# Optimization experiments

Hardware: AMD Instinct MI355X
Metric: run time of the kernel (lower is better)

Reference implementation:

```python
import jax, jax.numpy as jnp
import numpy as np

WS = 8      # window_size
NH = 3      # num_heads
SHIFT = True
LN_EPS = 1e-5


def _ln(x, w, b):
    m = jnp.mean(x, axis=-1, keepdims=True)
    v = jnp.mean(jnp.square(x - m), axis=-1, keepdims=True)
    return (x - m) * jax.lax.rsqrt(v + LN_EPS) * w + b


def _window_partition(x):
    B, H, W, C = x.shape
    x = x.reshape(B, H // WS, WS, W // WS, WS, C)
    return x.transpose(0, 1, 3, 2, 4, 5).reshape(-1, WS * WS, C)


def _window_reverse(win, B, H, W):
    C = win.shape[-1]
    x = win.reshape(B, H // WS, W // WS, WS, WS, C)
    return x.transpose(0, 1, 3, 2, 4, 5).reshape(B, H, W, C)


def setup_inputs() -> dict:
    key = jax.random.key(0)
    ks = jax.random.split(key, 6)
    C = 96
    x = jax.random.normal(ks[0], (4, 224, 224, C), dtype=jnp.float32)
    return {
        "x": x,
        "ln1_w": jnp.ones((C,), jnp.float32),
        "ln1_b": jnp.zeros((C,), jnp.float32),
        "in_proj_w": jax.random.normal(ks[1], (3 * C, C), jnp.float32) * 0.02,
        "in_proj_b": jnp.zeros((3 * C,), jnp.float32),
        "out_proj_w": jax.random.normal(ks[2], (C, C), jnp.float32) * 0.02,
        "out_proj_b": jnp.zeros((C,), jnp.float32),
        "ln2_w": jnp.ones((C,), jnp.float32),
        "ln2_b": jnp.zeros((C,), jnp.float32),
        "mlp_w1": jax.random.normal(ks[3], (4 * C, C), jnp.float32) * 0.02,
        "mlp_b1": jnp.zeros((4 * C,), jnp.float32),
        "mlp_w2": jax.random.normal(ks[4], (C, 4 * C), jnp.float32) * 0.02,
        "mlp_b2": jnp.zeros((C,), jnp.float32),
    }


def reference(x, ln1_w, ln1_b, in_proj_w, in_proj_b, out_proj_w, out_proj_b,
              ln2_w, ln2_b, mlp_w1, mlp_b1, mlp_w2, mlp_b2):
    B, H, W, C = x.shape
    hd = C // NH
    s = WS // 2
    if SHIFT:
        x = jnp.roll(x, shift=(-s, -s), axis=(1, 2))
    xw = _window_partition(x)                      # [nw, WS*WS, C]
    h = _ln(xw, ln1_w, ln1_b)
    qkv = h @ in_proj_w.T + in_proj_b              # [nw, L, 3C]
    q, k, v = jnp.split(qkv, 3, axis=-1)
    nw, L = q.shape[0], q.shape[1]
    q = q.reshape(nw, L, NH, hd).transpose(0, 2, 1, 3)
    k = k.reshape(nw, L, NH, hd).transpose(0, 2, 1, 3)
    v = v.reshape(nw, L, NH, hd).transpose(0, 2, 1, 3)
    scores = jnp.einsum('whqd,whkd->whqk', q, k) * (1.0 / np.sqrt(hd))
    attn = jax.nn.softmax(scores, axis=-1)
    o = jnp.einsum('whqk,whkd->whqd', attn, v).transpose(0, 2, 1, 3).reshape(nw, L, C)
    o = o @ out_proj_w.T + out_proj_b
    x = _window_reverse(o, B, H, W)                # attention REPLACES x (no residual, per source)
    if SHIFT:
        x = jnp.roll(x, shift=(s, s), axis=(1, 2))
    h2 = _ln(x, ln2_w, ln2_b)
    mlp = jax.nn.gelu(h2 @ mlp_w1.T + mlp_b1, approximate=False) @ mlp_w2.T + mlp_b2
    return x + mlp
```

## Files before the change

### kernel.cpp

```cpp
#include <hip/hip_runtime.h>
#include <math.h>

static constexpr int Hn   = 224;
static constexpr int Wn   = 224;
static constexpr int Cn   = 96;
static constexpr int Sft  = 4;
static constexpr int NWH  = 28;
static constexpr int NWPB = 784;
static constexpr int NW   = 3136;

typedef __attribute__((ext_vector_type(8))) short bf16x8;
typedef __attribute__((ext_vector_type(4))) float f32x4;
typedef __attribute__((ext_vector_type(4))) short s16x4;

__device__ inline short f2bf(float f) {
    unsigned u = __float_as_uint(f);
    return (short)((u + 0x7fffu + ((u >> 16) & 1u)) >> 16);
}

__device__ inline float gelu_f(float a) {
    float u  = a * 0.70710678118654752f;
    float au = fabsf(u);
    float t  = __builtin_amdgcn_rcpf(fmaf(0.3275911f, au, 1.f));
    float e  = __expf(-u * u);
    float p  = t * fmaf(t, fmaf(t, fmaf(t, fmaf(t, 1.061405429f,
                        -1.453152027f), 1.421413741f), -0.284496736f),
                        0.254829592f);
    float er = fmaf(-p, e, 1.f);
    er = (u < 0.f) ? -er : er;
    return 0.5f * a * (1.f + er);
}

__global__ void prep_bf16(const float* __restrict__ wqkv, const float* __restrict__ wo,
                          const float* __restrict__ w1,   const float* __restrict__ w2,
                          short* __restrict__ ws) {
    int idx = blockIdx.x * 256 + threadIdx.x;
    if (idx < 27648)        ws[idx] = f2bf(wqkv[idx]);
    else if (idx < 36864)   ws[idx] = f2bf(wo[idx - 27648]);
    else if (idx < 73728)   ws[idx] = f2bf(w1[idx - 36864]);
    else if (idx < 110592)  ws[idx] = f2bf(w2[idx - 73728]);
}

static constexpr int LDH  = 104;
static constexpr int LDQK = 200;
static constexpr int LDVT = 72;
static constexpr int LDP  = 200;
static constexpr int LDXF = 100;
static constexpr int LDST = 100;
static constexpr int LDAQ = 104;

__global__ __launch_bounds__(256) __attribute__((amdgpu_waves_per_eu(4, 4)))
void attn_mlp(
    const float* __restrict__ x,
    const float* __restrict__ ln1w, const float* __restrict__ ln1b,
    const short* __restrict__ wqb,  const float* __restrict__ bqkv,
    const short* __restrict__ wob,  const float* __restrict__ bo,
    const float* __restrict__ ln2w, const float* __restrict__ ln2b,
    const short* __restrict__ w1b,  const float* __restrict__ b1,
    const short* __restrict__ w2b,  const float* __restrict__ b2,
    float* __restrict__ out)
{
    __shared__ __align__(16) char  A[64 * 400];
    __shared__ __align__(16) short Bsh[96 * LDVT];
    __shared__ int   tbase[64];

    const int blk = blockIdx.x;
    const int b   = blk / NWPB;
    const int rem = blk - b * NWPB;
    const int wh  = rem / NWH;
    const int ww  = rem - wh * NWH;
    const int tid  = threadIdx.x;
    const int lane = tid & 63;
    const int wv   = __builtin_amdgcn_readfirstlane(tid >> 6);
    const int lr   = lane & 15;
    const int lk   = lane >> 4;
    const int wr   = wv >> 1;
    const int wc   = wv & 1;

    if (tid < 64) {
        int i = tid >> 3, j = tid & 7;
        int hs = wh * 8 + i + Sft; if (hs >= Hn) hs -= Hn;
        int ws2 = ww * 8 + j + Sft; if (ws2 >= Wn) ws2 -= Wn;
        tbase[tid] = ((b * Hn + hs) * Wn + ws2) * Cn;
    }
    __syncthreads();

    float* xf = (float*)A;
    for (int i = tid; i < 64 * 24; i += 256) {
        int row = i / 24, c4 = i - row * 24;
        float4 v = ((const float4*)(x + tbase[row]))[c4];
        *(float4*)&xf[row * LDXF + c4 * 4] = v;
    }
    __syncthreads();

    {
        short* lnb = Bsh;
        const int l = tid >> 2, p = tid & 3;
        float s0 = 0.f, s1 = 0.f;
        #pragma unroll
        for (int c0 = 0; c0 < 24; ++c0) {
            float v = xf[l * LDXF + p * 24 + c0];
            s0 += v; s1 += v * v;
        }
        s0 += __shfl_xor(s0, 1); s1 += __shfl_xor(s1, 1);
        s0 += __shfl_xor(s0, 2); s1 += __shfl_xor(s1, 2);
        float mean = s0 * (1.f / 96.f);
        float var  = fmaxf(s1 * (1.f / 96.f) - mean * mean, 0.f);
        float rstd = rsqrtf(var + 1e-5f);
        #pragma unroll
        for (int c0 = 0; c0 < 24; ++c0) {
            int c = p * 24 + c0;
            float v = xf[l * LDXF + c];
            lnb[l * LDH + c] = f2bf((v - mean) * rstd * ln1w[c] + ln1b[c]);
        }
    }
    __syncthreads();

    short* qk = (short*)A;
    short* vt = Bsh;
    {
        bf16x8 aq[2][3];
        #pragma unroll
        for (int rt = 0; rt < 2; ++rt)
            #pragma unroll
            for (int ks = 0; ks < 3; ++ks)
                aq[rt][ks] = *(const bf16x8*)&Bsh[(wr * 32 + rt * 16 + lr) * LDH + ks * 32 + lk * 8];
        __syncthreads();

        #pragma unroll 3
        for (int ct9 = 0; ct9 < 9; ++ct9) {
            const int ct = wc * 9 + ct9;
            const short* bp = wqb + (ct * 16 + lr) * 96 + lk * 8;
            bf16x8 b0 = *(const bf16x8*)(bp);
            bf16x8 b1 = *(const bf16x8*)(bp + 32);
            bf16x8 b2v = *(const bf16x8*)(bp + 64);
            const int col  = ct * 16 + lr;
            const float bs = bqkv[col];
            #pragma unroll
            for (int rt = 0; rt < 2; ++rt) {
                f32x4 acc = (f32x4){0.f, 0.f, 0.f, 0.f};
                acc = __builtin_amdgcn_mfma_f32_16x16x32_bf16(aq[rt][0], b0, acc, 0, 0, 0);
                acc = __builtin_amdgcn_mfma_f32_16x16x32_bf16(aq[rt][1], b1, acc, 0, 0, 0);
                acc = __builtin_amdgcn_mfma_f32_16x16x32_bf16(aq[rt][2], b2v, acc, 0, 0, 0);
                const int rb = wr * 32 + rt * 16;
                if (ct < 12) {
                    #pragma unroll
                    for (int r = 0; r < 4; ++r)
                        qk[(rb + lk * 4 + r) * LDQK + col] = f2bf(acc[r] + bs);
                } else {
                    s16x4 pk;
                    #pragma unroll
                    for (int r = 0; r < 4; ++r) pk[r] = f2bf(acc[r] + bs);
                    *(s16x4*)&vt[(col - 192) * LDVT + rb + lk * 4] = pk;
                }
            }
        }
    }
    __syncthreads();

    short* pb = (short*)A;
    {
        f32x4 accs[3][4];
        #pragma unroll
        for (int h = 0; h < 3; ++h) {
            bf16x8 aqf = *(const bf16x8*)&qk[(wv * 16 + lr) * LDQK + h * 32 + lk * 8];
            #pragma unroll
            for (int ct = 0; ct < 4; ++ct) {
                bf16x8 bk = *(const bf16x8*)&qk[(ct * 16 + lr) * LDQK + 96 + h * 32 + lk * 8];
                f32x4 z = (f32x4){0.f, 0.f, 0.f, 0.f};
                accs[h][ct] = __builtin_amdgcn_mfma_f32_16x16x32_bf16(aqf, bk, z, 0, 0, 0);
            }
        }
        __syncthreads();

        const float scale = 0.17677669529663687f;
        float inv[3][4];
        #pragma unroll
        for (int h = 0; h < 3; ++h) {
            #pragma unroll
            for (int r = 0; r < 4; ++r) {
                float m = fmaxf(fmaxf(accs[h][0][r], accs[h][1][r]),
                                fmaxf(accs[h][2][r], accs[h][3][r]));
                m = fmaxf(m, __shfl_xor(m, 1));
                m = fmaxf(m, __shfl_xor(m, 2));
                m = fmaxf(m, __shfl_xor(m, 4));
                m = fmaxf(m, __shfl_xor(m, 8));
                float s = 0.f;
                #pragma unroll
                for (int ct = 0; ct < 4; ++ct) {
                    float p = __expf((accs[h][ct][r] - m) * scale);
                    accs[h][ct][r] = p; s += p;
                }
                s += __shfl_xor(s, 1); s += __shfl_xor(s, 2);
                s += __shfl_xor(s, 4); s += __shfl_xor(s, 8);
                inv[h][r] = 1.f / s;
            }
        }
        #pragma unroll
        for (int h = 0; h < 3; ++h)
            #pragma unroll
            for (int ct = 0; ct < 4; ++ct)
                #pragma unroll
                for (int r = 0; r < 4; ++r)
                    pb[(wv * 16 + lk * 4 + r) * LDP + h * 64 + ct * 16 + lr] =
                        f2bf(accs[h][ct][r]);

        f32x4 acco[3][2];
        #pragma unroll
        for (int h = 0; h < 3; ++h)
            #pragma unroll
            for (int ct = 0; ct < 2; ++ct) acco[h][ct] = (f32x4){0.f, 0.f, 0.f, 0.f};
        #pragma unroll
        for (int h = 0; h < 3; ++h) {
            #pragma unroll
            for (int ks = 0; ks < 2; ++ks) {
                bf16x8 ap = *(const bf16x8*)&pb[(wv * 16 + lr) * LDP + h * 64 + ks * 32 + lk * 8];
                #pragma unroll
                for (int ct = 0; ct < 2; ++ct) {
                    bf16x8 bv = *(const bf16x8*)&vt[(h * 32 + ct * 16 + lr) * LDVT + ks * 32 + lk * 8];
                    acco[h][ct] = __builtin_amdgcn_mfma_f32_16x16x32_bf16(ap, bv, acco[h][ct], 0, 0, 0);
                }
            }
        }
        #pragma unroll
        for (int h = 0; h < 3; ++h)
            #pragma unroll
            for (int ct = 0; ct < 2; ++ct)
                #pragma unroll
                for (int r = 0; r < 4; ++r)
                    pb[(wv * 16 + lk * 4 + r) * LDP + h * 32 + ct * 16 + lr] =
                        f2bf(acco[h][ct][r] * inv[h][r]);
    }

    float* st = (float*)A;
    {
        bf16x8 o0 = *(const bf16x8*)&pb[(wv * 16 + lr) * LDP +  0 + lk * 8];
        bf16x8 o1 = *(const bf16x8*)&pb[(wv * 16 + lr) * LDP + 32 + lk * 8];
        bf16x8 o2 = *(const bf16x8*)&pb[(wv * 16 + lr) * LDP + 64 + lk * 8];
        #pragma unroll
        for (int ct = 0; ct < 6; ++ct) {
            const short* bp = wob + (ct * 16 + lr) * 96 + lk * 8;
            bf16x8 b0 = *(const bf16x8*)(bp);
            bf16x8 b1 = *(const bf16x8*)(bp + 32);
            bf16x8 b2v = *(const bf16x8*)(bp + 64);
            f32x4 acc = (f32x4){0.f, 0.f, 0.f, 0.f};
            acc = __builtin_amdgcn_mfma_f32_16x16x32_bf16(o0, b0, acc, 0, 0, 0);
            acc = __builtin_amdgcn_mfma_f32_16x16x32_bf16(o1, b1, acc, 0, 0, 0);
            acc = __builtin_amdgcn_mfma_f32_16x16x32_bf16(o2, b2v, acc, 0, 0, 0);
            const int col = ct * 16 + lr;
            const float bs = bo[col];
            #pragma unroll
            for (int r = 0; r < 4; ++r)
                st[(wv * 16 + lk * 4 + r) * LDST + col] = acc[r] + bs;
        }
    }
    __syncthreads();

    {
        short* lnb = Bsh;
        const int l = tid >> 2, p = tid & 3;
        float s0 = 0.f, s1 = 0.f;
        #pragma unroll
        for (int c0 = 0; c0 < 24; ++c0) {
            float v = st[l * LDST + p * 24 + c0];
            s0 += v; s1 += v * v;
        }
        s0 += __shfl_xor(s0, 1); s1 += __shfl_xor(s1, 1);
        s0 += __shfl_xor(s0, 2); s1 += __shfl_xor(s1, 2);
        float mean = s0 * (1.f / 96.f);
        float var  = fmaxf(s1 * (1.f / 96.f) - mean * mean, 0.f);
        float rstd = rsqrtf(var + 1e-5f);
        #pragma unroll
        for (int c0 = 0; c0 < 24; ++c0) {
            int c = p * 24 + c0;
            float v = st[l * LDST + c];
            lnb[l * LDH + c] = f2bf((v - mean) * rstd * ln2w[c] + ln2b[c]);
        }
    }
    __syncthreads();

    short* actQ = Bsh;
    bf16x8 a1[4][3];
    #pragma unroll
    for (int rt = 0; rt < 4; ++rt)
        #pragma unroll
        for (int ks = 0; ks < 3; ++ks)
            a1[rt][ks] = *(const bf16x8*)&Bsh[(rt * 16 + lr) * LDH + ks * 32 + lk * 8];
    __syncthreads();

    for (int half = 0; half < 2; ++half) {
        const int oc0w = half * 192 + wv * 48;
        f32x4 acc1[4][3];
        #pragma unroll
        for (int rt = 0; rt < 4; ++rt)
            #pragma unroll
            for (int ct = 0; ct < 3; ++ct) acc1[rt][ct] = (f32x4){0.f, 0.f, 0.f, 0.f};

        #pragma unroll
        for (int ct = 0; ct < 3; ++ct) {
            const short* bp = w1b + (oc0w + ct * 16 + lr) * 96 + lk * 8;
            bf16x8 bg0 = *(const bf16x8*)(bp);
            bf16x8 bg1 = *(const bf16x8*)(bp + 32);
            bf16x8 bg2 = *(const bf16x8*)(bp + 64);
            #pragma unroll
            for (int rt = 0; rt < 4; ++rt) {
                acc1[rt][ct] = __builtin_amdgcn_mfma_f32_16x16x32_bf16(a1[rt][0], bg0, acc1[rt][ct], 0, 0, 0);
                acc1[rt][ct] = __builtin_amdgcn_mfma_f32_16x16x32_bf16(a1[rt][1], bg1, acc1[rt][ct], 0, 0, 0);
                acc1[rt][ct] = __builtin_amdgcn_mfma_f32_16x16x32_bf16(a1[rt][2], bg2, acc1[rt][ct], 0, 0, 0);
            }
        }

        for (int sub = 0; sub < 2; ++sub) {
            if (wr == sub) {
                #pragma unroll
                for (int ct = 0; ct < 3; ++ct) {
                    float bias = b1[oc0w + ct * 16 + lr];
                    const int lcol = wc * 48 + ct * 16 + lr;
                    #pragma unroll
                    for (int rt = 0; rt < 4; ++rt) {
                        #pragma unroll
                        for (int r = 0; r < 4; ++r) {
                            float g = gelu_f(acc1[rt][ct][r] + bias);
                            actQ[(rt * 16 + lk * 4 + r) * LDAQ + lcol] = f2bf(g);
                        }
                    }
                }
            }
            __syncthreads();

            {
                f32x4 ps[2][3];
                #pragma unroll
                for (int rt = 0; rt < 2; ++rt)
                    #pragma unroll
                    for (int ct = 0; ct < 3; ++ct) ps[rt][ct] = (f32x4){0.f, 0.f, 0.f, 0.f};

                #pragma unroll
                for (int ks = 0; ks < 3; ++ks) {
                    bf16x8 a2[2];
                    #pragma unroll
                    for (int rt = 0; rt < 2; ++rt)
                        a2[rt] = *(const bf16x8*)&actQ[(wr * 32 + rt * 16 + lr) * LDAQ + ks * 32 + lk * 8];
                    #pragma unroll
                    for (int ct = 0; ct < 3; ++ct) {
                        bf16x8 bw = *(const bf16x8*)(w2b + (wc * 48 + ct * 16 + lr) * 384
                                                      + half * 192 + sub * 96 + ks * 32 + lk * 8);
                        #pragma unroll
                        for (int rt = 0; rt < 2; ++rt)
                            ps[rt][ct] = __builtin_amdgcn_mfma_f32_16x16x32_bf16(a2[rt], bw, ps[rt][ct], 0, 0, 0);
                    }
                }

                const bool last = (half == 1) && (sub == 1);
                #pragma unroll
                for (int ct = 0; ct < 3; ++ct) {
                    const int col = wc * 48 + ct * 16 + lr;
                    const float addb = last ? b2[col] : 0.f;
                    #pragma unroll
                    for (int rt = 0; rt < 2; ++rt) {
                        #pragma unroll
                        for (int r = 0; r < 4; ++r) {
                            const int row = wr * 32 + rt * 16 + lk * 4 + r;
                            st[row * LDST + col] += ps[rt][ct][r] + addb;
                        }
                    }
                }
            }
            __syncthreads();
        }
    }

    for (int i = tid; i < 64 * 96; i += 256) {
        int l = i / 96, c = i - l * 96;
        out[tbase[l] + c] = st[l * LDST + c];
    }
}

extern "C" void kernel_launch(void* const* d_in, const int* in_sizes, int n_in,
                              void* d_out, int out_size, void* d_ws, size_t ws_size,
                              hipStream_t stream) {
    const float* x    = (const float*)d_in[0];
    const float* ln1w = (const float*)d_in[1];
    const float* ln1b = (const float*)d_in[2];
    const float* wqkv = (const float*)d_in[3];
    const float* bqkv = (const float*)d_in[4];
    const float* wo   = (const float*)d_in[5];
    const float* bo   = (const float*)d_in[6];
    const float* ln2w = (const float*)d_in[7];
    const float* ln2b = (const float*)d_in[8];
    const float* w1   = (const float*)d_in[9];
    const float* b1   = (const float*)d_in[10];
    const float* w2   = (const float*)d_in[11];
    const float* b2   = (const float*)d_in[12];
    float* out = (float*)d_out;

    short* ws  = (short*)d_ws;
    short* wqb = ws;
    short* wob = ws + 27648;
    short* w1b = ws + 36864;
    short* w2b = ws + 73728;

    prep_bf16<<<432, 256, 0, stream>>>(wqkv, wo, w1, w2, ws);
    attn_mlp<<<NW, 256, 0, stream>>>(x, ln1w, ln1b, wqb, bqkv, wob, bo,
                                     ln2w, ln2b, w1b, b1, w2b, b2, out);
}
```

Measured before the change: 223.6 us.

## Restructure MLP so each wave owns 16 rows, removing block barriers

The MLP stage now gives each wave its own 16 token rows and a private LDS scratch region. The wave computes the full fc1 output for 192 columns per half, applies GELU, and runs fc2 with register accumulators across both halves. This removes the shared activation buffer and the several __syncthreads per half, and adds the residual to st only once at the end. In exchange each wave reloads all W1 and W2 weights, so global and L2 weight traffic goes up fourfold. LDS grows and the launch bounds change from a fixed 4 waves per EU to a minimum of 3 blocks, which can change occupancy.

```diff
diff --git a/kernel.cpp b/kernel.cpp
--- a/kernel.cpp
+++ b/kernel.cpp
@@ -47,10 +47,9 @@
 static constexpr int LDP  = 200;
 static constexpr int LDXF = 100;
 static constexpr int LDST = 100;
-static constexpr int LDAQ = 104;
-
-__global__ __launch_bounds__(256) __attribute__((amdgpu_waves_per_eu(4, 4)))
-void attn_mlp(
+static constexpr int LDM  = 200;
+
+__global__ __launch_bounds__(256, 3) void attn_mlp(
     const float* __restrict__ x,
     const float* __restrict__ ln1w, const float* __restrict__ ln1b,
     const short* __restrict__ wqb,  const float* __restrict__ bqkv,
@@ -61,7 +60,7 @@
     float* __restrict__ out)
 {
     __shared__ __align__(16) char  A[64 * 400];
-    __shared__ __align__(16) short Bsh[96 * LDVT];
+    __shared__ __align__(16) short Bsh[12800];
     __shared__ int   tbase[64];
 
     const int blk = blockIdx.x;
@@ -256,9 +255,12 @@
     }
     __syncthreads();
 
-    {
-        short* lnb = Bsh;
-        const int l = tid >> 2, p = tid & 3;
+    short* Mw = Bsh + wv * (16 * LDM);
+
+    {
+        const int l   = tid >> 2;
+        const int lr2 = lane >> 2;
+        const int p   = tid & 3;
         float s0 = 0.f, s1 = 0.f;
         #pragma unroll
         for (int c0 = 0; c0 < 24; ++c0) {
@@ -274,101 +276,67 @@
         for (int c0 = 0; c0 < 24; ++c0) {
             int c = p * 24 + c0;
             float v = st[l * LDST + c];
-            lnb[l * LDH + c] = f2bf((v - mean) * rstd * ln2w[c] + ln2b[c]);
-        }
-    }
-    __syncthreads();
-
-    short* actQ = Bsh;
-    bf16x8 a1[4][3];
+            Mw[lr2 * LDM + c] = f2bf((v - mean) * rstd * ln2w[c] + ln2b[c]);
+        }
+    }
+
+    bf16x8 a1[3];
     #pragma unroll
-    for (int rt = 0; rt < 4; ++rt)
-        #pragma unroll
-        for (int ks = 0; ks < 3; ++ks)
-            a1[rt][ks] = *(const bf16x8*)&Bsh[(rt * 16 + lr) * LDH + ks * 32 + lk * 8];
-    __syncthreads();
+    for (int ks = 0; ks < 3; ++ks)
+        a1[ks] = *(const bf16x8*)&Mw[lr * LDM + ks * 32 + lk * 8];
+
+    f32x4 acc2[6];
+    #pragma unroll
+    for (int ct = 0; ct < 6; ++ct) acc2[ct] = (f32x4){0.f, 0.f, 0.f, 0.f};
 
     for (int half = 0; half < 2; ++half) {
-        const int oc0w = half * 192 + wv * 48;
-        f32x4 acc1[4][3];
-        #pragma unroll
-        for (int rt = 0; rt < 4; ++rt)
-            #pragma unroll
-            for (int ct = 0; ct < 3; ++ct) acc1[rt][ct] = (f32x4){0.f, 0.f, 0.f, 0.f};
-
-        #pragma unroll
-        for (int ct = 0; ct < 3; ++ct) {
-            const short* bp = w1b + (oc0w + ct * 16 + lr) * 96 + lk * 8;
+        f32x4 acc1[12];
+        #pragma unroll
+        for (int ct = 0; ct < 12; ++ct) acc1[ct] = (f32x4){0.f, 0.f, 0.f, 0.f};
+        #pragma unroll
+        for (int ct = 0; ct < 12; ++ct) {
+            const short* bp = w1b + (half * 192 + ct * 16 + lr) * 96 + lk * 8;
             bf16x8 bg0 = *(const bf16x8*)(bp);
             bf16x8 bg1 = *(const bf16x8*)(bp + 32);
             bf16x8 bg2 = *(const bf16x8*)(bp + 64);
-            #pragma unroll
-            for (int rt = 0; rt < 4; ++rt) {
-                acc1[rt][ct] = __builtin_amdgcn_mfma_f32_16x16x32_bf16(a1[rt][0], bg0, acc1[rt][ct], 0, 0, 0);
-                acc1[rt][ct] = __builtin_amdgcn_mfma_f32_16x16x32_bf16(a1[rt][1], bg1, acc1[rt][ct], 0, 0, 0);
-                acc1[rt][ct] = __builtin_amdgcn_mfma_f32_16x16x32_bf16(a1[rt][2], bg2, acc1[rt][ct], 0, 0, 0);
-            }
-        }
-
-        for (int sub = 0; sub < 2; ++sub) {
-            if (wr == sub) {
-                #pragma unroll
-                for (int ct = 0; ct < 3; ++ct) {
-                    float bias = b1[oc0w + ct * 16 + lr];
-                    const int lcol = wc * 48 + ct * 16 + lr;
-                    #pragma unroll
-                    for (int rt = 0; rt < 4; ++rt) {
-                        #pragma unroll
-                        for (int r = 0; r < 4; ++r) {
-                            float g = gelu_f(acc1[rt][ct][r] + bias);
-                            actQ[(rt * 16 + lk * 4 + r) * LDAQ + lcol] = f2bf(g);
-                        }
-                    }
-                }
-            }
-            __syncthreads();
-
-            {
-                f32x4 ps[2][3];
-                #pragma unroll
-                for (int rt = 0; rt < 2; ++rt)
-                    #pragma unroll
-                    for (int ct = 0; ct < 3; ++ct) ps[rt][ct] = (f32x4){0.f, 0.f, 0.f, 0.f};
-
-                #pragma unroll
-                for (int ks = 0; ks < 3; ++ks) {
-                    bf16x8 a2[2];
-                    #pragma unroll
-                    for (int rt = 0; rt < 2; ++rt)
-                        a2[rt] = *(const bf16x8*)&actQ[(wr * 32 + rt * 16 + lr) * LDAQ + ks * 32 + lk * 8];
-                    #pragma unroll
-                    for (int ct = 0; ct < 3; ++ct) {
-                        bf16x8 bw = *(const bf16x8*)(w2b + (wc * 48 + ct * 16 + lr) * 384
-                                                      + half * 192 + sub * 96 + ks * 32 + lk * 8);
-                        #pragma unroll
-                        for (int rt = 0; rt < 2; ++rt)
-                            ps[rt][ct] = __builtin_amdgcn_mfma_f32_16x16x32_bf16(a2[rt], bw, ps[rt][ct], 0, 0, 0);
-                    }
-                }
-
-                const bool last = (half == 1) && (sub == 1);
-                #pragma unroll
-                for (int ct = 0; ct < 3; ++ct) {
-                    const int col = wc * 48 + ct * 16 + lr;
-                    const float addb = last ? b2[col] : 0.f;
-                    #pragma unroll
-                    for (int rt = 0; rt < 2; ++rt) {
-                        #pragma unroll
-                        for (int r = 0; r < 4; ++r) {
-                            const int row = wr * 32 + rt * 16 + lk * 4 + r;
-                            st[row * LDST + col] += ps[rt][ct][r] + addb;
-                        }
-                    }
-                }
-            }
-            __syncthreads();
-        }
-    }
+            acc1[ct] = __builtin_amdgcn_mfma_f32_16x16x32_bf16(a1[0], bg0, acc1[ct], 0, 0, 0);
+            acc1[ct] = __builtin_amdgcn_mfma_f32_16x16x32_bf16(a1[1], bg1, acc1[ct], 0, 0, 0);
+            acc1[ct] = __builtin_amdgcn_mfma_f32_16x16x32_bf16(a1[2], bg2, acc1[ct], 0, 0, 0);
+        }
+
+        #pragma unroll
+        for (int ct = 0; ct < 12; ++ct) {
+            const float bias = b1[half * 192 + ct * 16 + lr];
+            #pragma unroll
+            for (int r = 0; r < 4; ++r) {
+                float g = gelu_f(acc1[ct][r] + bias);
+                Mw[(lk * 4 + r) * LDM + ct * 16 + lr] = f2bf(g);
+            }
+        }
+
+        #pragma unroll
+        for (int ks = 0; ks < 6; ++ks) {
+            bf16x8 a2 = *(const bf16x8*)&Mw[lr * LDM + ks * 32 + lk * 8];
+            #pragma unroll
+            for (int ct = 0; ct < 6; ++ct) {
+                bf16x8 bw = *(const bf16x8*)(w2b + (ct * 16 + lr) * 384
+                                              + half * 192 + ks * 32 + lk * 8);
+                acc2[ct] = __builtin_amdgcn_mfma_f32_16x16x32_bf16(a2, bw, acc2[ct], 0, 0, 0);
+            }
+        }
+    }
+
+    #pragma unroll
+    for (int ct = 0; ct < 6; ++ct) {
+        const int col = ct * 16 + lr;
+        const float bias = b2[col];
+        #pragma unroll
+        for (int r = 0; r < 4; ++r) {
+            const int row = wv * 16 + lk * 4 + r;
+            st[row * LDST + col] += acc2[ct][r] + bias;
+        }
+    }
+    __syncthreads();
 
     for (int i = tid; i < 64 * 96; i += 256) {
         int l = i / 96, c = i - l * 96;
```

Result: slower. 250.2 us (+11.9%).
